# Optimization experiments

Measured on AMD Instinct MI355X. Metric: run time of the kernel, lower is better.

## Reference

```python
import jax, jax.numpy as jnp
import numpy as np

N = 4096
D = 256
H = 8
E = 131072
NEG = -1e30  # stands in for -inf; keeps grads NaN-free


def setup_inputs() -> dict:
    key = jax.random.key(0)
    ks = jax.random.split(key, 8)
    s = 1.0 / np.sqrt(D)
    return {
        "x": jax.random.normal(ks[0], (N, D), dtype=jnp.float32),
        "edge_index": jax.random.randint(ks[1], (2, E), 0, N, dtype=jnp.int32),
        "Wq": jax.random.normal(ks[2], (D, D), dtype=jnp.float32) * s,
        "Wk": jax.random.normal(ks[3], (D, D), dtype=jnp.float32) * s,
        "Wv": jax.random.normal(ks[4], (D, D), dtype=jnp.float32) * s,
        "Wo": jax.random.normal(ks[5], (D, D), dtype=jnp.float32) * s,
        "bo": jnp.zeros((D,), dtype=jnp.float32),
        "gamma": jnp.ones((D,), dtype=jnp.float32),
        "beta": jnp.zeros((D,), dtype=jnp.float32),
    }


def reference(x, edge_index, Wq, Wk, Wv, Wo, bo, gamma, beta):
    n, d_model = x.shape
    d_h = d_model // H
    scale = jnp.sqrt(jnp.float32(d_h))

    # mask: True = blocked. Diagonal and graph edges (dst attends to src) unblocked.
    mask = jnp.ones((n, n), dtype=bool)
    diag = jnp.arange(n)
    mask = mask.at[diag, diag].set(False)
    src, dst = edge_index[0], edge_index[1]
    mask = mask.at[dst, src].set(False)

    # projections: torch Linear computes x @ W.T
    Q = (x @ Wq.T).reshape(n, H, d_h).transpose(1, 0, 2)  # [H, N, d_h]
    K = (x @ Wk.T).reshape(n, H, d_h).transpose(1, 0, 2)
    V = (x @ Wv.T).reshape(n, H, d_h).transpose(1, 0, 2)

    scores = jnp.einsum("hnd,hmd->hnm", Q, K) / scale      # [H, N, N]
    scores = jnp.where(mask[None, :, :], NEG, scores)
    attn = jax.nn.softmax(scores, axis=-1)
    attn = jnp.nan_to_num(attn, nan=0.0)

    out = jnp.einsum("hnm,hmd->hnd", attn, V)              # [H, N, d_h]
    out = out.transpose(1, 0, 2).reshape(n, d_model)
    out = out @ Wo.T + bo

    # LayerNorm(x + out), eps=1e-5
    h = x + out
    mu = jnp.mean(h, axis=-1, keepdims=True)
    var = jnp.var(h, axis=-1, keepdims=True)
    return (h - mu) * jax.lax.rsqrt(var + 1e-5) * gamma + beta
```

## Files before the change

### kernel.cpp

```cpp
#include <hip/hip_runtime.h>

#define D_MODEL 256
#define N_HEADS 8
#define MAXN 128
#define NGEMM 384

typedef __attribute__((ext_vector_type(8))) short bf16x8;
typedef __attribute__((ext_vector_type(4))) float f32x4;

__device__ __forceinline__ unsigned short f2bf(float f) {
    union { float f; unsigned int u; } v; v.f = f;
    unsigned int r = v.u + 0x7fff + ((v.u >> 16) & 1);
    return (unsigned short)(r >> 16);
}
__device__ __forceinline__ float bf2f(unsigned short u) {
    union { unsigned int u; float f; } v; v.u = ((unsigned int)u) << 16;
    return v.f;
}

__global__ void prep_kernel(const float* __restrict__ x,
                            const float* __restrict__ W0, const float* __restrict__ W1,
                            const float* __restrict__ W2, const float* __restrict__ W3,
                            unsigned short* __restrict__ xb,
                            unsigned short* __restrict__ O0, unsigned short* __restrict__ O1,
                            unsigned short* __restrict__ O2, unsigned short* __restrict__ O3,
                            unsigned long long* __restrict__ mask, int n) {
    const int XV = (4096 * 256) / 4;
    int i = blockIdx.x * blockDim.x + threadIdx.x;

    int wpr = n >> 6;
    int mwords = n * wpr;
    if (i < mwords) {
        int row = i >> 6;
        int w = i & 63;
        mask[i] = (w == (row >> 6)) ? (1ULL << (row & 63)) : 0ULL;
    }

    const float* src;
    unsigned short* dst;
    int k;
    if (i < XV) {
        src = x; dst = xb; k = i;
    } else {
        int i2 = i - XV;
        if (i2 >= 4 * 16384) return;
        int z = i2 >> 14;
        k = i2 & 16383;
        src = (z == 0) ? W0 : (z == 1) ? W1 : (z == 2) ? W2 : W3;
        dst = (z == 0) ? O0 : (z == 1) ? O1 : (z == 2) ? O2 : O3;
    }
    float4 v = *(const float4*)(src + (size_t)k * 4);
    ushort4 o;
    o.x = f2bf(v.x); o.y = f2bf(v.y); o.z = f2bf(v.z); o.w = f2bf(v.w);
    *(ushort4*)(dst + (size_t)k * 4) = o;
}

__global__ __launch_bounds__(256) void qkv_edges_kernel(
        const unsigned short* __restrict__ xb,
        const unsigned short* __restrict__ Wq, const unsigned short* __restrict__ Wk,
        const unsigned short* __restrict__ Wv,
        unsigned short* __restrict__ Qb, unsigned short* __restrict__ Kb,
        unsigned short* __restrict__ Vb,
        const int* __restrict__ ei, unsigned long long* __restrict__ mask,
        int E, int n) {
    int blk = blockIdx.x;
    if (blk >= NGEMM) {
        int e = (blk - NGEMM) * 256 + threadIdx.x;
        if (e < E) {
            int src = ei[e];
            int dst = ei[E + e];
            int wpr = n >> 6;
            atomicOr(&mask[(size_t)dst * wpr + (src >> 6)], 1ULL << (src & 63));
        }
        return;
    }
    int z = blk >> 7;
    int r = blk & 127;
    int by = r >> 2, bx = r & 3;
    const unsigned short* B = (z == 0) ? Wq : (z == 1) ? Wk : Wv;
    unsigned short* Cb = (z == 0) ? Qb : (z == 1) ? Kb : Vb;

    __shared__ short Alds[128][72];
    __shared__ short Blds[64][72];
    int t = threadIdx.x;
    int wave = t >> 6, lane = t & 63;
    int wr = wave >> 1, wc = wave & 1;
    int lr = t >> 3;
    int lk = (t & 7) << 3;

    const unsigned short* Abase = xb + ((size_t)(by * 128 + lr)) * D_MODEL + lk;
    const unsigned short* Bbase = B + ((size_t)(bx * 64 + lr)) * D_MODEL + lk;

    int fm = lane & 15;
    int fk = (lane >> 4) << 3;

    f32x4 acc[4][2];
#pragma unroll
    for (int rr = 0; rr < 4; ++rr)
#pragma unroll
        for (int c = 0; c < 2; ++c) acc[rr][c] = (f32x4){0.f, 0.f, 0.f, 0.f};

    for (int k0 = 0; k0 < D_MODEL; k0 += 64) {
        *(uint4*)&Alds[lr][lk]      = *(const uint4*)(Abase + k0);
        *(uint4*)&Alds[lr + 32][lk] = *(const uint4*)(Abase + 32 * D_MODEL + k0);
        *(uint4*)&Alds[lr + 64][lk] = *(const uint4*)(Abase + 64 * D_MODEL + k0);
        *(uint4*)&Alds[lr + 96][lk] = *(const uint4*)(Abase + 96 * D_MODEL + k0);
        *(uint4*)&Blds[lr][lk]      = *(const uint4*)(Bbase + k0);
        *(uint4*)&Blds[lr + 32][lk] = *(const uint4*)(Bbase + 32 * D_MODEL + k0);
        __syncthreads();
#pragma unroll
        for (int ks = 0; ks < 64; ks += 32) {
            bf16x8 af[4], bf[2];
#pragma unroll
            for (int rr = 0; rr < 4; ++rr)
                af[rr] = *(const bf16x8*)&Alds[wr * 64 + rr * 16 + fm][ks + fk];
#pragma unroll
            for (int c = 0; c < 2; ++c)
                bf[c] = *(const bf16x8*)&Blds[wc * 32 + c * 16 + fm][ks + fk];
#pragma unroll
            for (int rr = 0; rr < 4; ++rr)
#pragma unroll
                for (int c = 0; c < 2; ++c)
                    acc[rr][c] = __builtin_amdgcn_mfma_f32_16x16x32_bf16(
                        af[rr], bf[c], acc[rr][c], 0, 0, 0);
        }
        __syncthreads();
    }

    int orow0 = by * 128 + wr * 64 + ((lane >> 4) << 2);
    int ocol0 = bx * 64 + wc * 32 + (lane & 15);
#pragma unroll
    for (int rr = 0; rr < 4; ++rr)
#pragma unroll
        for (int c = 0; c < 2; ++c)
#pragma unroll
            for (int q = 0; q < 4; ++q)
                Cb[(size_t)(orow0 + rr * 16 + q) * D_MODEL + ocol0 + c * 16] =
                    f2bf(acc[rr][c][q]);
}

#define LOAD_K(KR, tt)                                                        \
    do {                                                                      \
        int _ti = (tt);                                                       \
        if (_ti < nt) {                                                       \
            int _ix = nbr[_ti * 16 + col];                                    \
            const unsigned short* _kr = Kb + _ix * D_MODEL + (kq << 3);       \
            KR[0] = *(const bf16x8*)(_kr + 0 * 32);                           \
            KR[1] = *(const bf16x8*)(_kr + 1 * 32);                           \
            KR[2] = *(const bf16x8*)(_kr + 2 * 32);                           \
            KR[3] = *(const bf16x8*)(_kr + 3 * 32);                           \
            KR[4] = *(const bf16x8*)(_kr + 4 * 32);                           \
            KR[5] = *(const bf16x8*)(_kr + 5 * 32);                           \
            KR[6] = *(const bf16x8*)(_kr + 6 * 32);                           \
            KR[7] = *(const bf16x8*)(_kr + 7 * 32);                           \
        }                                                                     \
    } while (0)

#define FMA4(P, W, V)                                                         \
    do {                                                                      \
        P[0] += (W) * bf2f((unsigned short)((V).x & 0xffff));                 \
        P[1] += (W) * bf2f((unsigned short)((V).x >> 16));                    \
        P[2] += (W) * bf2f((unsigned short)((V).y & 0xffff));                 \
        P[3] += (W) * bf2f((unsigned short)((V).y >> 16));                    \
    } while (0)

#define TILE_BODY(KC, KN, tt)                                                 \
    do {                                                                      \
        int _t = (tt);                                                        \
        int _b0 = _t << 4;                                                    \
                                 \
        int4 _i0 = *(const int4*)&nbr[_b0];                                   \
        int4 _i1 = *(const int4*)&nbr[_b0 + 4];                               \
        int4 _i2 = *(const int4*)&nbr[_b0 + 8];                               \
        int4 _i3 = *(const int4*)&nbr[_b0 + 12];                              \
          \
        uint2 _v0  = *(const uint2*)(vbase + _i0.x * D_MODEL);                \
        uint2 _v1  = *(const uint2*)(vbase + _i0.y * D_MODEL);                \
        uint2 _v2  = *(const uint2*)(vbase + _i0.z * D_MODEL);                \
        uint2 _v3  = *(const uint2*)(vbase + _i0.w * D_MODEL);                \
        uint2 _v4  = *(const uint2*)(vbase + _i1.x * D_MODEL);                \
        uint2 _v5  = *(const uint2*)(vbase + _i1.y * D_MODEL);                \
        uint2 _v6  = *(const uint2*)(vbase + _i1.z * D_MODEL);                \
        uint2 _v7  = *(const uint2*)(vbase + _i1.w * D_MODEL);                \
        uint2 _v8  = *(const uint2*)(vbase + _i2.x * D_MODEL);                \
        uint2 _v9  = *(const uint2*)(vbase + _i2.y * D_MODEL);                \
        uint2 _v10 = *(const uint2*)(vbase + _i2.z * D_MODEL);                \
        uint2 _v11 = *(const uint2*)(vbase + _i2.w * D_MODEL);                \
        uint2 _v12 = *(const uint2*)(vbase + _i3.x * D_MODEL);                \
        uint2 _v13 = *(const uint2*)(vbase + _i3.y * D_MODEL);                \
        uint2 _v14 = *(const uint2*)(vbase + _i3.z * D_MODEL);                \
        uint2 _v15 = *(const uint2*)(vbase + _i3.w * D_MODEL);                \
                          \
        LOAD_K(KN, _t + 1);                                                   \
                 \
        f32x4 _c0 = (f32x4){0.f, 0.f, 0.f, 0.f};                              \
        f32x4 _c1 = (f32x4){0.f, 0.f, 0.f, 0.f};                              \
        _c0 = __builtin_amdgcn_mfma_f32_16x16x32_bf16(KC[0], (col == 0) ? qf : zf, _c0, 0, 0, 0); \
        _c1 = __builtin_amdgcn_mfma_f32_16x16x32_bf16(KC[1], (col == 1) ? qf : zf, _c1, 0, 0, 0); \
        _c0 = __builtin_amdgcn_mfma_f32_16x16x32_bf16(KC[2], (col == 2) ? qf : zf, _c0, 0, 0, 0); \
        _c1 = __builtin_amdgcn_mfma_f32_16x16x32_bf16(KC[3], (col == 3) ? qf : zf, _c1, 0, 0, 0); \
        _c0 = __builtin_amdgcn_mfma_f32_16x16x32_bf16(KC[4], (col == 4) ? qf : zf, _c0, 0, 0, 0); \
        _c1 = __builtin_amdgcn_mfma_f32_16x16x32_bf16(KC[5], (col == 5) ? qf : zf, _c1, 0, 0, 0); \
        _c0 = __builtin_amdgcn_mfma_f32_16x16x32_bf16(KC[6], (col == 6) ? qf : zf, _c0, 0, 0, 0); \
        _c1 = __builtin_amdgcn_mfma_f32_16x16x32_bf16(KC[7], (col == 7) ? qf : zf, _c1, 0, 0, 0); \
        float _s0 = (_c0[0] + _c1[0]) * inv_scale;                            \
        float _s1 = (_c0[1] + _c1[1]) * inv_scale;                            \
        float _s2 = (_c0[2] + _c1[2]) * inv_scale;                            \
        float _s3 = (_c0[3] + _c1[3]) * inv_scale;                            \
        int _jr = _b0 + (kq << 2);                                            \
        _s0 = (_jr + 0 < cnt) ? _s0 : -1e30f;                                 \
        _s1 = (_jr + 1 < cnt) ? _s1 : -1e30f;                                 \
        _s2 = (_jr + 2 < cnt) ? _s2 : -1e30f;                                 \
        _s3 = (_jr + 3 < cnt) ? _s3 : -1e30f;                                 \
        \
        float _mt = fmaxf(fmaxf(_s0, _s1), fmaxf(_s2, _s3));                  \
        _mt = fmaxf(_mt, __shfl_xor(_mt, 16, 64));                            \
        _mt = fmaxf(_mt, __shfl_xor(_mt, 32, 64));                            \
        float _w0 = __expf(_s0 - _mt);                                        \
        float _w1 = __expf(_s1 - _mt);                                        \
        float _w2 = __expf(_s2 - _mt);                                        \
        float _w3 = __expf(_s3 - _mt);                                        \
        float _ts = (_w0 + _w1) + (_w2 + _w3);                                \
        _ts += __shfl_xor(_ts, 16, 64);                                       \
        _ts += __shfl_xor(_ts, 32, 64);                                       \
                       \
        float _mh = __shfl(_mt, h, 64);                                       \
        float _th = __shfl(_ts, h, 64);                                       \
        float _mn = fmaxf(m, _mh);                                            \
        float _so = __expf(m - _mn);                                          \
        float _f  = __expf(_mh - _mn);                                        \
        m = _mn;                                                              \
        l = l * _so + _th * _f;                                               \
             \
        f32x4 _p = (f32x4){0.f, 0.f, 0.f, 0.f};                               \
        {                                                                     \
            float _wa = __shfl(_w0, h, 64), _wb = __shfl(_w1, h, 64);         \
            float _wc = __shfl(_w2, h, 64), _wd = __shfl(_w3, h, 64);         \
            FMA4(_p, _wa, _v0); FMA4(_p, _wb, _v1);                           \
            FMA4(_p, _wc, _v2); FMA4(_p, _wd, _v3);                           \
        }                                                                     \
        {                                                                     \
            float _wa = __shfl(_w0, h + 16, 64), _wb = __shfl(_w1, h + 16, 64); \
            float _wc = __shfl(_w2, h + 16, 64), _wd = __shfl(_w3, h + 16, 64); \
            FMA4(_p, _wa, _v4); FMA4(_p, _wb, _v5);                           \
            FMA4(_p, _wc, _v6); FMA4(_p, _wd, _v7);                           \
        }                                                                     \
        {                                                                     \
            float _wa = __shfl(_w0, h + 32, 64), _wb = __shfl(_w1, h + 32, 64); \
            float _wc = __shfl(_w2, h + 32, 64), _wd = __shfl(_w3, h + 32, 64); \
            FMA4(_p, _wa, _v8); FMA4(_p, _wb, _v9);                           \
            FMA4(_p, _wc, _v10); FMA4(_p, _wd, _v11);                         \
        }                                                                     \
        {                                                                     \
            float _wa = __shfl(_w0, h + 48, 64), _wb = __shfl(_w1, h + 48, 64); \
            float _wc = __shfl(_w2, h + 48, 64), _wd = __shfl(_w3, h + 48, 64); \
            FMA4(_p, _wa, _v12); FMA4(_p, _wb, _v13);                         \
            FMA4(_p, _wc, _v14); FMA4(_p, _wd, _v15);                         \
        }                                                                     \
        acc[0] = acc[0] * _so + _p[0] * _f;                                   \
        acc[1] = acc[1] * _so + _p[1] * _f;                                   \
        acc[2] = acc[2] * _so + _p[2] * _f;                                   \
        acc[3] = acc[3] * _so + _p[3] * _f;                                   \
    } while (0)

__global__ __launch_bounds__(64) void attn_kernel(
        const unsigned short* __restrict__ Qb, const unsigned short* __restrict__ Kb,
        const unsigned short* __restrict__ Vb,
        const unsigned long long* __restrict__ mask,
        unsigned short* __restrict__ Ob, int n) {
    int dst = blockIdx.x;
    int L = threadIdx.x;
    int wpr = n >> 6;

    __shared__ alignas(16) int nbr[MAXN + 16];

    unsigned long long w = (L < wpr) ? mask[(size_t)dst * wpr + L] : 0ULL;
    int c = __popcll(w);
    int xs = c;
#pragma unroll
    for (int o = 1; o < 64; o <<= 1) {
        int y = __shfl_up(xs, o, 64);
        if (L >= o) xs += y;
    }
    int pos = xs - c;
    while (w) {
        int b = __builtin_ctzll(w);
        w &= w - 1;
        if (pos < MAXN) nbr[pos] = (L << 6) + b;
        ++pos;
    }
    int cnt = __shfl(xs, 63, 64);
    if (cnt > MAXN) cnt = MAXN;
    int nb = (cnt + 15) & ~15;
    __syncthreads();
    int last = nbr[cnt - 1];
    if (L < nb - cnt) nbr[cnt + L] = last;
    __syncthreads();
    int nt = nb >> 4;

    int col = L & 15;
    int kq = L >> 4;
    bf16x8 qf = (bf16x8){0, 0, 0, 0, 0, 0, 0, 0};
    if (col < N_HEADS)
        qf = *(const bf16x8*)(Qb + (size_t)dst * D_MODEL + col * 32 + kq * 8);
    const bf16x8 zf = (bf16x8){0, 0, 0, 0, 0, 0, 0, 0};
    const float inv_scale = 0.17677669529663687f;

    int h = L >> 3;
    const unsigned short* vbase = Vb + 4 * L;

    float m = -1e30f, l = 0.f;
    f32x4 acc = (f32x4){0.f, 0.f, 0.f, 0.f};

    bf16x8 KA[8], KBx[8];
    LOAD_K(KA, 0);
    for (int t = 0; t < nt; t += 2) {
        TILE_BODY(KA, KBx, t);
        if (t + 1 < nt) TILE_BODY(KBx, KA, t + 1);
    }

    float rl = 1.f / l;
    ushort4 o;
    o.x = f2bf(acc[0] * rl); o.y = f2bf(acc[1] * rl);
    o.z = f2bf(acc[2] * rl); o.w = f2bf(acc[3] * rl);
    *(ushort4*)(Ob + (size_t)dst * D_MODEL + 4 * L) = o;
}

struct SMemO {
    union {
        struct { short A[32][72]; short B[256][72]; } st;
        float c[32][260];
    };
};

__global__ __launch_bounds__(256) void gemm_o_ln_kernel(
        const unsigned short* __restrict__ Ob, const unsigned short* __restrict__ Wob,
        const float* __restrict__ x, const float* __restrict__ bo,
        const float* __restrict__ gamma, const float* __restrict__ beta,
        float* __restrict__ out) {
    __shared__ SMemO sm;
    int by = blockIdx.x;
    int t = threadIdx.x;
    int wave = t >> 6, lane = t & 63;
    int rt = wave >> 1, cq = wave & 1;
    int lr = t >> 3;
    int lk = (t & 7) << 3;

    const unsigned short* Abase = Ob + ((size_t)(by * 32 + lr)) * D_MODEL + lk;
    int fm = lane & 15;
    int fk = (lane >> 4) << 3;

    f32x4 acc[8];
#pragma unroll
    for (int ct = 0; ct < 8; ++ct) acc[ct] = (f32x4){0.f, 0.f, 0.f, 0.f};

    for (int k0 = 0; k0 < D_MODEL; k0 += 64) {
        *(uint4*)&sm.st.A[lr][lk] = *(const uint4*)(Abase + k0);
#pragma unroll
        for (int j = 0; j < 8; ++j)
            *(uint4*)&sm.st.B[lr + 32 * j][lk] =
                *(const uint4*)(Wob + ((size_t)(lr + 32 * j)) * D_MODEL + k0 + lk);
        __syncthreads();
#pragma unroll
        for (int ks = 0; ks < 64; ks += 32) {
            bf16x8 af = *(const bf16x8*)&sm.st.A[rt * 16 + fm][ks + fk];
#pragma unroll
            for (int ct = 0; ct < 8; ++ct) {
                bf16x8 bf = *(const bf16x8*)&sm.st.B[cq * 128 + ct * 16 + fm][ks + fk];
                acc[ct] = __builtin_amdgcn_mfma_f32_16x16x32_bf16(af, bf, acc[ct], 0, 0, 0);
            }
        }
        __syncthreads();
    }

    int rr0 = rt * 16 + ((lane >> 4) << 2);
#pragma unroll
    for (int ct = 0; ct < 8; ++ct)
#pragma unroll
        for (int q = 0; q < 4; ++q)
            sm.c[rr0 + q][cq * 128 + ct * 16 + (lane & 15)] = acc[ct][q];
    __syncthreads();

    float4 bo4 = *(const float4*)(bo + lane * 4);
    float4 g4  = *(const float4*)(gamma + lane * 4);
    float4 be4 = *(const float4*)(beta + lane * 4);
#pragma unroll
    for (int rr = 0; rr < 8; ++rr) {
        int r = wave * 8 + rr;
        int grow = by * 32 + r;
        float4 p = *(const float4*)&sm.c[r][lane * 4];
        float4 xv = *(const float4*)(x + (size_t)grow * D_MODEL + lane * 4);
        float hx = p.x + xv.x + bo4.x;
        float hy = p.y + xv.y + bo4.y;
        float hz = p.z + xv.z + bo4.z;
        float hw = p.w + xv.w + bo4.w;
        float s  = (hx + hy) + (hz + hw);
        float s2 = (hx * hx + hy * hy) + (hz * hz + hw * hw);
#pragma unroll
        for (int o = 32; o; o >>= 1) {
            s  += __shfl_xor(s, o, 64);
            s2 += __shfl_xor(s2, o, 64);
        }
        float mu = s * (1.f / 256.f);
        float var = s2 * (1.f / 256.f) - mu * mu;
        float rstd = rsqrtf(var + 1e-5f);
        float4 o4;
        o4.x = (hx - mu) * rstd * g4.x + be4.x;
        o4.y = (hy - mu) * rstd * g4.y + be4.y;
        o4.z = (hz - mu) * rstd * g4.z + be4.z;
        o4.w = (hw - mu) * rstd * g4.w + be4.w;
        *(float4*)(out + (size_t)grow * D_MODEL + lane * 4) = o4;
    }
}

extern "C" void kernel_launch(void* const* d_in, const int* in_sizes, int n_in,
                              void* d_out, int out_size, void* d_ws, size_t ws_size,
                              hipStream_t stream) {
    const float* x     = (const float*)d_in[0];
    const int*   ei    = (const int*)  d_in[1];
    const float* Wq    = (const float*)d_in[2];
    const float* Wk    = (const float*)d_in[3];
    const float* Wv    = (const float*)d_in[4];
    const float* Wo    = (const float*)d_in[5];
    const float* bo    = (const float*)d_in[6];
    const float* gamma = (const float*)d_in[7];
    const float* beta  = (const float*)d_in[8];
    float* out = (float*)d_out;

    int n = in_sizes[0] / D_MODEL;
    int E = in_sizes[1] / 2;

    char* ws = (char*)d_ws;
    size_t off = 0;
    unsigned long long* mask = (unsigned long long*)(ws + off);
    off += (size_t)n * (n >> 6) * sizeof(unsigned long long);
    unsigned short* xb  = (unsigned short*)(ws + off); off += (size_t)n * D_MODEL * 2;
    unsigned short* Wqb = (unsigned short*)(ws + off); off += D_MODEL * D_MODEL * 2;
    unsigned short* Wkb = (unsigned short*)(ws + off); off += D_MODEL * D_MODEL * 2;
    unsigned short* Wvb = (unsigned short*)(ws + off); off += D_MODEL * D_MODEL * 2;
    unsigned short* Wob = (unsigned short*)(ws + off); off += D_MODEL * D_MODEL * 2;
    unsigned short* Qb  = (unsigned short*)(ws + off); off += (size_t)n * D_MODEL * 2;
    unsigned short* Kb  = (unsigned short*)(ws + off); off += (size_t)n * D_MODEL * 2;
    unsigned short* Vb  = (unsigned short*)(ws + off); off += (size_t)n * D_MODEL * 2;
    unsigned short* Ob  = (unsigned short*)(ws + off); off += (size_t)n * D_MODEL * 2;

    prep_kernel<<<1280, 256, 0, stream>>>(x, Wq, Wk, Wv, Wo,
                                          xb, Wqb, Wkb, Wvb, Wob, mask, n);

    int edge_blocks = (E + 255) / 256;
    qkv_edges_kernel<<<NGEMM + edge_blocks, 256, 0, stream>>>(
        xb, Wqb, Wkb, Wvb, Qb, Kb, Vb, ei, mask, E, n);

    attn_kernel<<<n, 64, 0, stream>>>(Qb, Kb, Vb, mask, Ob, n);

    gemm_o_ln_kernel<<<n / 32, 256, 0, stream>>>(Ob, Wob, x, bo, gamma, beta, out);
}
```

Baseline: 115.8 us.

## Fuse x bf16 conversion into QKV GEMM, shrink tiles, use LDS for attention weights

The fp32-to-bf16 conversion of x moves out of the prep kernel and into the QKV GEMM's shared-memory load, which removes the xb intermediate buffer and its round trip through memory. The QKV GEMM and the output-projection/LayerNorm GEMM use smaller row tiles (64 and 16 rows), doubling their grid sizes to fill more compute units. In the attention kernel, per-head softmax weights and the running max/sum now go through shared memory instead of many cross-lane shuffles. Smaller tiles reload the weight matrices more often, and the shared-memory exchange relies on single-wave ordering without explicit barriers.

```diff
diff --git a/kernel.cpp b/kernel.cpp
--- a/kernel.cpp
+++ b/kernel.cpp
@@ -3,7 +3,7 @@
 #define D_MODEL 256
 #define N_HEADS 8
 #define MAXN 128
-#define NGEMM 384
+#define NGEMM 768
 
 typedef __attribute__((ext_vector_type(8))) short bf16x8;
 typedef __attribute__((ext_vector_type(4))) float f32x4;
@@ -18,14 +18,11 @@
     return v.f;
 }
 
-__global__ void prep_kernel(const float* __restrict__ x,
-                            const float* __restrict__ W0, const float* __restrict__ W1,
+__global__ void prep_kernel(const float* __restrict__ W0, const float* __restrict__ W1,
                             const float* __restrict__ W2, const float* __restrict__ W3,
-                            unsigned short* __restrict__ xb,
                             unsigned short* __restrict__ O0, unsigned short* __restrict__ O1,
                             unsigned short* __restrict__ O2, unsigned short* __restrict__ O3,
                             unsigned long long* __restrict__ mask, int n) {
-    const int XV = (4096 * 256) / 4;
     int i = blockIdx.x * blockDim.x + threadIdx.x;
 
     int wpr = n >> 6;
@@ -35,28 +32,20 @@
         int w = i & 63;
         mask[i] = (w == (row >> 6)) ? (1ULL << (row & 63)) : 0ULL;
     }
-
-    const float* src;
-    unsigned short* dst;
-    int k;
-    if (i < XV) {
-        src = x; dst = xb; k = i;
-    } else {
-        int i2 = i - XV;
-        if (i2 >= 4 * 16384) return;
-        int z = i2 >> 14;
-        k = i2 & 16383;
-        src = (z == 0) ? W0 : (z == 1) ? W1 : (z == 2) ? W2 : W3;
-        dst = (z == 0) ? O0 : (z == 1) ? O1 : (z == 2) ? O2 : O3;
-    }
-    float4 v = *(const float4*)(src + (size_t)k * 4);
-    ushort4 o;
-    o.x = f2bf(v.x); o.y = f2bf(v.y); o.z = f2bf(v.z); o.w = f2bf(v.w);
-    *(ushort4*)(dst + (size_t)k * 4) = o;
+    if (i < 4 * 16384) {
+        int z = i >> 14;
+        int k = i & 16383;
+        const float* src = (z == 0) ? W0 : (z == 1) ? W1 : (z == 2) ? W2 : W3;
+        unsigned short* dst = (z == 0) ? O0 : (z == 1) ? O1 : (z == 2) ? O2 : O3;
+        float4 v = *(const float4*)(src + (size_t)k * 4);
+        ushort4 o;
+        o.x = f2bf(v.x); o.y = f2bf(v.y); o.z = f2bf(v.z); o.w = f2bf(v.w);
+        *(ushort4*)(dst + (size_t)k * 4) = o;
+    }
 }
 
 __global__ __launch_bounds__(256) void qkv_edges_kernel(
-        const unsigned short* __restrict__ xb,
+        const float* __restrict__ x,
         const unsigned short* __restrict__ Wq, const unsigned short* __restrict__ Wk,
         const unsigned short* __restrict__ Wv,
         unsigned short* __restrict__ Qb, unsigned short* __restrict__ Kb,
@@ -74,63 +63,72 @@
         }
         return;
     }
-    int z = blk >> 7;
-    int r = blk & 127;
+    int z = blk >> 8;
+    int r = blk & 255;
     int by = r >> 2, bx = r & 3;
     const unsigned short* B = (z == 0) ? Wq : (z == 1) ? Wk : Wv;
     unsigned short* Cb = (z == 0) ? Qb : (z == 1) ? Kb : Vb;
 
-    __shared__ short Alds[128][72];
+    __shared__ short Alds[64][72];
     __shared__ short Blds[64][72];
     int t = threadIdx.x;
     int wave = t >> 6, lane = t & 63;
     int wr = wave >> 1, wc = wave & 1;
-    int lr = t >> 3;
-    int lk = (t & 7) << 3;
-
-    const unsigned short* Abase = xb + ((size_t)(by * 128 + lr)) * D_MODEL + lk;
-    const unsigned short* Bbase = B + ((size_t)(bx * 64 + lr)) * D_MODEL + lk;
+    int sr = t >> 2;
+    int sc = (t & 3) << 4;
+
+    const float* Abase = x + (size_t)(by * 64 + sr) * D_MODEL + sc;
+    const unsigned short* Bbase = B + (size_t)(bx * 64 + sr) * D_MODEL + sc;
 
     int fm = lane & 15;
     int fk = (lane >> 4) << 3;
 
-    f32x4 acc[4][2];
-#pragma unroll
-    for (int rr = 0; rr < 4; ++rr)
+    f32x4 acc[2][2];
+#pragma unroll
+    for (int rr = 0; rr < 2; ++rr)
 #pragma unroll
         for (int c = 0; c < 2; ++c) acc[rr][c] = (f32x4){0.f, 0.f, 0.f, 0.f};
 
     for (int k0 = 0; k0 < D_MODEL; k0 += 64) {
-        *(uint4*)&Alds[lr][lk]      = *(const uint4*)(Abase + k0);
-        *(uint4*)&Alds[lr + 32][lk] = *(const uint4*)(Abase + 32 * D_MODEL + k0);
-        *(uint4*)&Alds[lr + 64][lk] = *(const uint4*)(Abase + 64 * D_MODEL + k0);
-        *(uint4*)&Alds[lr + 96][lk] = *(const uint4*)(Abase + 96 * D_MODEL + k0);
-        *(uint4*)&Blds[lr][lk]      = *(const uint4*)(Bbase + k0);
-        *(uint4*)&Blds[lr + 32][lk] = *(const uint4*)(Bbase + 32 * D_MODEL + k0);
+        float4 a0 = *(const float4*)(Abase + k0);
+        float4 a1 = *(const float4*)(Abase + k0 + 4);
+        float4 a2 = *(const float4*)(Abase + k0 + 8);
+        float4 a3 = *(const float4*)(Abase + k0 + 12);
+        ushort4 u0, u1, u2, u3;
+        u0.x = f2bf(a0.x); u0.y = f2bf(a0.y); u0.z = f2bf(a0.z); u0.w = f2bf(a0.w);
+        u1.x = f2bf(a1.x); u1.y = f2bf(a1.y); u1.z = f2bf(a1.z); u1.w = f2bf(a1.w);
+        u2.x = f2bf(a2.x); u2.y = f2bf(a2.y); u2.z = f2bf(a2.z); u2.w = f2bf(a2.w);
+        u3.x = f2bf(a3.x); u3.y = f2bf(a3.y); u3.z = f2bf(a3.z); u3.w = f2bf(a3.w);
+        *(ushort4*)&Alds[sr][sc]      = u0;
+        *(ushort4*)&Alds[sr][sc + 4]  = u1;
+        *(ushort4*)&Alds[sr][sc + 8]  = u2;
+        *(ushort4*)&Alds[sr][sc + 12] = u3;
+        *(uint4*)&Blds[sr][sc]     = *(const uint4*)(Bbase + k0);
+        *(uint4*)&Blds[sr][sc + 8] = *(const uint4*)(Bbase + k0 + 8);
         __syncthreads();
 #pragma unroll
         for (int ks = 0; ks < 64; ks += 32) {
-            bf16x8 af[4], bf[2];
-#pragma unroll
-            for (int rr = 0; rr < 4; ++rr)
-                af[rr] = *(const bf16x8*)&Alds[wr * 64 + rr * 16 + fm][ks + fk];
+            bf16x8 af[2], bfr[2];
+#pragma unroll
+            for (int rr = 0; rr < 2; ++rr)
+                af[rr] = *(const bf16x8*)&Alds[wr * 32 + rr * 16 + fm][ks + fk];
 #pragma unroll
             for (int c = 0; c < 2; ++c)
-                bf[c] = *(const bf16x8*)&Blds[wc * 32 + c * 16 + fm][ks + fk];
-#pragma unroll
-            for (int rr = 0; rr < 4; ++rr)
+                bfr[c] = *(const bf16x8*)&Blds[wc * 32 + c * 16 + fm][ks + fk];
+#pragma unroll
+            for (int rr = 0; rr < 2; ++rr)
 #pragma unroll
                 for (int c = 0; c < 2; ++c)
                     acc[rr][c] = __builtin_amdgcn_mfma_f32_16x16x32_bf16(
-                        af[rr], bf[c], acc[rr][c], 0, 0, 0);
+                        af[rr], bfr[c], acc[rr][c], 0, 0, 0);
         }
         __syncthreads();
     }
 
-    int orow0 = by * 128 + wr * 64 + ((lane >> 4) << 2);
+    int orow0 = by * 64 + wr * 32 + ((lane >> 4) << 2);
     int ocol0 = bx * 64 + wc * 32 + (lane & 15);
 #pragma unroll
-    for (int rr = 0; rr < 4; ++rr)
+    for (int rr = 0; rr < 2; ++rr)
 #pragma unroll
         for (int c = 0; c < 2; ++c)
 #pragma unroll
@@ -168,7 +166,6 @@
     do {                                                                      \
         int _t = (tt);                                                        \
         int _b0 = _t << 4;                                                    \
-                                 \
         int4 _i0 = *(const int4*)&nbr[_b0];                                   \
         int4 _i1 = *(const int4*)&nbr[_b0 + 4];                               \
         int4 _i2 = *(const int4*)&nbr[_b0 + 8];                               \
@@ -192,7 +189,6 @@
         uint2 _v15 = *(const uint2*)(vbase + _i3.w * D_MODEL);                \
                           \
         LOAD_K(KN, _t + 1);                                                   \
-                 \
         f32x4 _c0 = (f32x4){0.f, 0.f, 0.f, 0.f};                              \
         f32x4 _c1 = (f32x4){0.f, 0.f, 0.f, 0.f};                              \
         _c0 = __builtin_amdgcn_mfma_f32_16x16x32_bf16(KC[0], (col == 0) ? qf : zf, _c0, 0, 0, 0); \
@@ -212,7 +208,7 @@
         _s1 = (_jr + 1 < cnt) ? _s1 : -1e30f;                                 \
         _s2 = (_jr + 2 < cnt) ? _s2 : -1e30f;                                 \
         _s3 = (_jr + 3 < cnt) ? _s3 : -1e30f;                                 \
-        \
+           \
         float _mt = fmaxf(fmaxf(_s0, _s1), fmaxf(_s2, _s3));                  \
         _mt = fmaxf(_mt, __shfl_xor(_mt, 16, 64));                            \
         _mt = fmaxf(_mt, __shfl_xor(_mt, 32, 64));                            \
@@ -223,40 +219,32 @@
         float _ts = (_w0 + _w1) + (_w2 + _w3);                                \
         _ts += __shfl_xor(_ts, 16, 64);                                       \
         _ts += __shfl_xor(_ts, 32, 64);                                       \
-                       \
-        float _mh = __shfl(_mt, h, 64);                                       \
-        float _th = __shfl(_ts, h, 64);                                       \
-        float _mn = fmaxf(m, _mh);                                            \
+          \
+        if (col < N_HEADS) {                                                  \
+            float4 _wq; _wq.x = _w0; _wq.y = _w1; _wq.z = _w2; _wq.w = _w3;   \
+            *(float4*)&w_t[col][kq << 2] = _wq;                               \
+            if (kq == 0) { float2 _ax2; _ax2.x = _mt; _ax2.y = _ts;           \
+                           aux2[col] = _ax2; }                                \
+        }                                                                     \
+        float2 _ax = aux2[h];                                                 \
+        float _mn = fmaxf(m, _ax.x);                                          \
         float _so = __expf(m - _mn);                                          \
-        float _f  = __expf(_mh - _mn);                                        \
+        float _f  = __expf(_ax.x - _mn);                                      \
         m = _mn;                                                              \
-        l = l * _so + _th * _f;                                               \
-             \
+        l = l * _so + _ax.y * _f;                                             \
+        float4 _wA = *(const float4*)&w_t[h][0];                              \
+        float4 _wB = *(const float4*)&w_t[h][4];                              \
+        float4 _wC = *(const float4*)&w_t[h][8];                              \
+        float4 _wD = *(const float4*)&w_t[h][12];                             \
         f32x4 _p = (f32x4){0.f, 0.f, 0.f, 0.f};                               \
-        {                                                                     \
-            float _wa = __shfl(_w0, h, 64), _wb = __shfl(_w1, h, 64);         \
-            float _wc = __shfl(_w2, h, 64), _wd = __shfl(_w3, h, 64);         \
-            FMA4(_p, _wa, _v0); FMA4(_p, _wb, _v1);                           \
-            FMA4(_p, _wc, _v2); FMA4(_p, _wd, _v3);                           \
-        }                                                                     \
-        {                                                                     \
-            float _wa = __shfl(_w0, h + 16, 64), _wb = __shfl(_w1, h + 16, 64); \
-            float _wc = __shfl(_w2, h + 16, 64), _wd = __shfl(_w3, h + 16, 64); \
-            FMA4(_p, _wa, _v4); FMA4(_p, _wb, _v5);                           \
-            FMA4(_p, _wc, _v6); FMA4(_p, _wd, _v7);                           \
-        }                                                                     \
-        {                                                                     \
-            float _wa = __shfl(_w0, h + 32, 64), _wb = __shfl(_w1, h + 32, 64); \
-            float _wc = __shfl(_w2, h + 32, 64), _wd = __shfl(_w3, h + 32, 64); \
-            FMA4(_p, _wa, _v8); FMA4(_p, _wb, _v9);                           \
-            FMA4(_p, _wc, _v10); FMA4(_p, _wd, _v11);                         \
-        }                                                                     \
-        {                                                                     \
-            float _wa = __shfl(_w0, h + 48, 64), _wb = __shfl(_w1, h + 48, 64); \
-            float _wc = __shfl(_w2, h + 48, 64), _wd = __shfl(_w3, h + 48, 64); \
-            FMA4(_p, _wa, _v12); FMA4(_p, _wb, _v13);                         \
-            FMA4(_p, _wc, _v14); FMA4(_p, _wd, _v15);                         \
-        }                                                                     \
+        FMA4(_p, _wA.x, _v0);  FMA4(_p, _wA.y, _v1);                          \
+        FMA4(_p, _wA.z, _v2);  FMA4(_p, _wA.w, _v3);                          \
+        FMA4(_p, _wB.x, _v4);  FMA4(_p, _wB.y, _v5);                          \
+        FMA4(_p, _wB.z, _v6);  FMA4(_p, _wB.w, _v7);                          \
+        FMA4(_p, _wC.x, _v8);  FMA4(_p, _wC.y, _v9);                          \
+        FMA4(_p, _wC.z, _v10); FMA4(_p, _wC.w, _v11);                         \
+        FMA4(_p, _wD.x, _v12); FMA4(_p, _wD.y, _v13);                         \
+        FMA4(_p, _wD.z, _v14); FMA4(_p, _wD.w, _v15);                         \
         acc[0] = acc[0] * _so + _p[0] * _f;                                   \
         acc[1] = acc[1] * _so + _p[1] * _f;                                   \
         acc[2] = acc[2] * _so + _p[2] * _f;                                   \
@@ -273,6 +261,8 @@
     int wpr = n >> 6;
 
     __shared__ alignas(16) int nbr[MAXN + 16];
+    __shared__ float w_t[N_HEADS][20];
+    __shared__ float2 aux2[N_HEADS];
 
     unsigned long long w = (L < wpr) ? mask[(size_t)dst * wpr + L] : 0ULL;
     int c = __popcll(w);
@@ -328,8 +318,8 @@
 
 struct SMemO {
     union {
-        struct { short A[32][72]; short B[256][72]; } st;
-        float c[32][260];
+        struct { short A[16][72]; short B[256][72]; } st;
+        float c[16][260];
     };
 };
 
@@ -342,20 +332,21 @@
     int by = blockIdx.x;
     int t = threadIdx.x;
     int wave = t >> 6, lane = t & 63;
-    int rt = wave >> 1, cq = wave & 1;
+    int ar = t >> 4;
+    int ac = (t & 15) << 2;
     int lr = t >> 3;
     int lk = (t & 7) << 3;
 
-    const unsigned short* Abase = Ob + ((size_t)(by * 32 + lr)) * D_MODEL + lk;
+    const unsigned short* Abase = Ob + ((size_t)(by * 16 + ar)) * D_MODEL + ac;
     int fm = lane & 15;
     int fk = (lane >> 4) << 3;
 
-    f32x4 acc[8];
-#pragma unroll
-    for (int ct = 0; ct < 8; ++ct) acc[ct] = (f32x4){0.f, 0.f, 0.f, 0.f};
+    f32x4 acc[4];
+#pragma unroll
+    for (int ct = 0; ct < 4; ++ct) acc[ct] = (f32x4){0.f, 0.f, 0.f, 0.f};
 
     for (int k0 = 0; k0 < D_MODEL; k0 += 64) {
-        *(uint4*)&sm.st.A[lr][lk] = *(const uint4*)(Abase + k0);
+        *(ushort4*)&sm.st.A[ar][ac] = *(const ushort4*)(Abase + k0);
 #pragma unroll
         for (int j = 0; j < 8; ++j)
             *(uint4*)&sm.st.B[lr + 32 * j][lk] =
@@ -363,31 +354,31 @@
         __syncthreads();
 #pragma unroll
         for (int ks = 0; ks < 64; ks += 32) {
-            bf16x8 af = *(const bf16x8*)&sm.st.A[rt * 16 + fm][ks + fk];
-#pragma unroll
-            for (int ct = 0; ct < 8; ++ct) {
-                bf16x8 bf = *(const bf16x8*)&sm.st.B[cq * 128 + ct * 16 + fm][ks + fk];
-                acc[ct] = __builtin_amdgcn_mfma_f32_16x16x32_bf16(af, bf, acc[ct], 0, 0, 0);
+            bf16x8 af = *(const bf16x8*)&sm.st.A[fm][ks + fk];
+#pragma unroll
+            for (int ct = 0; ct < 4; ++ct) {
+                bf16x8 bfr = *(const bf16x8*)&sm.st.B[wave * 64 + ct * 16 + fm][ks + fk];
+                acc[ct] = __builtin_amdgcn_mfma_f32_16x16x32_bf16(af, bfr, acc[ct], 0, 0, 0);
             }
         }
         __syncthreads();
     }
 
-    int rr0 = rt * 16 + ((lane >> 4) << 2);
-#pragma unroll
-    for (int ct = 0; ct < 8; ++ct)
+    int rr0 = (lane >> 4) << 2;
+#pragma unroll
+    for (int ct = 0; ct < 4; ++ct)
 #pragma unroll
         for (int q = 0; q < 4; ++q)
-            sm.c[rr0 + q][cq * 128 + ct * 16 + (lane & 15)] = acc[ct][q];
+            sm.c[rr0 + q][wave * 64 + ct * 16 + (lane & 15)] = acc[ct][q];
     __syncthreads();
 
     float4 bo4 = *(const float4*)(bo + lane * 4);
     float4 g4  = *(const float4*)(gamma + lane * 4);
     float4 be4 = *(const float4*)(beta + lane * 4);
 #pragma unroll
-    for (int rr = 0; rr < 8; ++rr) {
-        int r = wave * 8 + rr;
-        int grow = by * 32 + r;
+    for (int rr = 0; rr < 4; ++rr) {
+        int r = wave * 4 + rr;
+        int grow = by * 16 + r;
         float4 p = *(const float4*)&sm.c[r][lane * 4];
         float4 xv = *(const float4*)(x + (size_t)grow * D_MODEL + lane * 4);
         float hx = p.x + xv.x + bo4.x;
@@ -434,7 +425,6 @@
     size_t off = 0;
     unsigned long long* mask = (unsigned long long*)(ws + off);
     off += (size_t)n * (n >> 6) * sizeof(unsigned long long);
-    unsigned short* xb  = (unsigned short*)(ws + off); off += (size_t)n * D_MODEL * 2;
     unsigned short* Wqb = (unsigned short*)(ws + off); off += D_MODEL * D_MODEL * 2;
     unsigned short* Wkb = (unsigned short*)(ws + off); off += D_MODEL * D_MODEL * 2;
     unsigned short* Wvb = (unsigned short*)(ws + off); off += D_MODEL * D_MODEL * 2;
@@ -444,14 +434,15 @@
     unsigned short* Vb  = (unsigned short*)(ws + off); off += (size_t)n * D_MODEL * 2;
     unsigned short* Ob  = (unsigned short*)(ws + off); off += (size_t)n * D_MODEL * 2;
 
-    prep_kernel<<<1280, 256, 0, stream>>>(x, Wq, Wk, Wv, Wo,
-                                          xb, Wqb, Wkb, Wvb, Wob, mask, n);
+    int mwords = n * (n >> 6);
+    prep_kernel<<<(mwords + 255) / 256, 256, 0, stream>>>(
+        Wq, Wk, Wv, Wo, Wqb, Wkb, Wvb, Wob, mask, n);
 
     int edge_blocks = (E + 255) / 256;
     qkv_edges_kernel<<<NGEMM + edge_blocks, 256, 0, stream>>>(
-        xb, Wqb, Wkb, Wvb, Qb, Kb, Vb, ei, mask, E, n);
+        x, Wqb, Wkb, Wvb, Qb, Kb, Vb, ei, mask, E, n);
 
     attn_kernel<<<n, 64, 0, stream>>>(Qb, Kb, Vb, mask, Ob, n);
 
-    gemm_o_ln_kernel<<<n / 32, 256, 0, stream>>>(Ob, Wob, x, bo, gamma, beta, out);
-}
+    gemm_o_ln_kernel<<<n / 16, 256, 0, stream>>>(Ob, Wob, x, bo, gamma, beta, out);
+}
```

After: 121.7 us. 5.1% more time.
